# Performance work log

Hardware: AMD Instinct MI355X
Metric: run time of the kernel (lower is better)

## Reference

```python
import jax, jax.numpy as jnp
import numpy as np

NUM_HEADS = 16


def setup_inputs() -> dict:
    rng = jax.random.key(0)
    ks = jax.random.split(rng, 11)
    T, B, E = 1024, 4, 1024
    s = E ** -0.5  # weight init scale
    return {
        "query": jax.random.normal(ks[0], (T, B, E), jnp.float32),
        "key": jax.random.normal(ks[1], (T, B, E), jnp.float32),
        "value": jax.random.normal(ks[2], (T, B, E), jnp.float32),
        "q_proj_weight": jax.random.normal(ks[3], (E, E), jnp.float32) * s,
        "k_proj_weight1": jax.random.normal(ks[4], (E, E), jnp.float32) * s,
        "k_proj_weight2": jax.random.normal(ks[5], (E, E), jnp.float32) * s,
        "v_proj_weight": jax.random.normal(ks[6], (E, E), jnp.float32) * s,
        "in_proj_bias": jax.random.normal(ks[7], (4 * E,), jnp.float32) * 0.02,
        "out_proj_weight": jax.random.normal(ks[8], (E, E), jnp.float32) * s,
        "out_proj_bias": jax.random.normal(ks[9], (E,), jnp.float32) * 0.02,
        "pi": jax.random.uniform(ks[10], (2, NUM_HEADS), jnp.float32, 0.3, 0.7),
    }


def reference(query, key, value, q_proj_weight, k_proj_weight1, k_proj_weight2,
              v_proj_weight, in_proj_bias, out_proj_weight, out_proj_bias, pi):
    T, Bz, E = query.shape
    H = NUM_HEADS
    hd = E // H
    scaling = hd ** -0.5

    b_q, b_k1, b_k2, b_v = jnp.split(in_proj_bias, 4)
    q = query @ q_proj_weight.T + b_q
    k1 = key @ k_proj_weight1.T + b_k1
    k2 = key @ k_proj_weight2.T + b_k2
    v = value @ v_proj_weight.T + b_v

    def heads(x):  # (S, B, E) -> (B*H, S, hd)
        S = x.shape[0]
        return x.reshape(S, Bz * H, hd).transpose(1, 0, 2)

    q, k1, k2, v = heads(q), heads(k1), heads(k2), heads(v)

    def sqdist(a, b):  # (B*H, Nt, hd), (B*H, Ns, hd) -> (B*H, Nt, Ns)
        a2 = jnp.sum(a * a, axis=-1)
        b2 = jnp.sum(b * b, axis=-1)
        ab = jnp.einsum('btd,bsd->bts', a, b)
        return a2[:, :, None] + b2[:, None, :] - 2.0 * ab

    e1 = jnp.exp(-scaling / 2.0 * sqdist(q, k1))
    e2 = jnp.exp(-3.0 * scaling / 2.0 * sqdist(q, k2))

    pi1 = jnp.clip(jnp.abs(pi[0]), 1e-6, 2.0)  # (H,)
    pi2 = jnp.clip(jnp.abs(pi[1]), 1e-6, 2.0)

    Nt, Ns = e1.shape[1], e1.shape[2]
    attn = (e1.reshape(Bz, H, Nt, Ns) * pi1[None, :, None, None]
            + e2.reshape(Bz, H, Nt, Ns) * pi2[None, :, None, None])
    attn = attn.reshape(Bz * H, Nt, Ns)
    attn = attn / (jnp.sum(attn, axis=-1, keepdims=True) + 1e-6)

    out = jnp.einsum('bts,bsd->btd', attn, v)        # (B*H, Nt, hd)
    out = out.transpose(1, 0, 2).reshape(T, Bz, E)   # (T, B, E)
    return out @ out_proj_weight.T + out_proj_bias
```

## Files before the change

### kernel.cpp

```cpp
#include <hip/hip_runtime.h>
#include <hip/hip_bf16.h>

#define T_DIM 1024
#define B_DIM 4
#define E_DIM 1024
#define H_DIM 16
#define HD    64
#define M_DIM (T_DIM * B_DIM)

typedef __hip_bfloat16 bf16;
typedef __bf16 bf16x8 __attribute__((ext_vector_type(8)));
typedef __bf16 bf16x4 __attribute__((ext_vector_type(4)));
typedef float  f32x4  __attribute__((ext_vector_type(4)));

#define P4S ((size_t)M_DIM * E_DIM)
#define P1S ((size_t)E_DIM * E_DIM)

__global__ __launch_bounds__(256) void cvt_all(
    const float* __restrict__ q, const float* __restrict__ k,
    const float* __restrict__ v, const float* __restrict__ w0,
    const float* __restrict__ w1, const float* __restrict__ w2,
    const float* __restrict__ w3, const float* __restrict__ w4,
    __bf16* __restrict__ dst)
{
  size_t i = ((size_t)blockIdx.x * 256 + threadIdx.x) * 8;
  const float* src;
  size_t off;
  if (i < P4S)            { src = q; off = i; }
  else if (i < 2 * P4S)   { src = k; off = i - P4S; }
  else if (i < 3 * P4S)   { src = v; off = i - 2 * P4S; }
  else {
    size_t j = i - 3 * P4S;
    int wsel = (int)(j >> 20);
    off = j & (P1S - 1);
    const float* ws[5] = {w0, w1, w2, w3, w4};
    src = ws[wsel];
  }
  float4 a = *(const float4*)(src + off);
  float4 b = *(const float4*)(src + off + 4);
  bf16x8 o;
  o[0] = (__bf16)a.x; o[1] = (__bf16)a.y; o[2] = (__bf16)a.z; o[3] = (__bf16)a.w;
  o[4] = (__bf16)b.x; o[5] = (__bf16)b.y; o[6] = (__bf16)b.z; o[7] = (__bf16)b.w;
  *(bf16x8*)(dst + i) = o;
}

__device__ __forceinline__ void load_lds16(const __bf16* g, __bf16* l) {
  __builtin_amdgcn_global_load_lds(
      (__attribute__((address_space(1))) void*)(void*)g,
      (__attribute__((address_space(3))) void*)l, 16, 0, 0);
}

template <typename TO>
__device__ __forceinline__ void gemm_body(
    const __bf16* __restrict__ X, const __bf16* __restrict__ W,
    const float* __restrict__ bias, TO* __restrict__ C,
    int bm, int bn, int Ndim, int Kdim, __bf16* As, __bf16* Bs)
{
  const int tid  = threadIdx.x;
  const int lane = tid & 63;
  const int wave = tid >> 6;
  const int wy = (wave >> 1) * 64;
  const int wx = (wave & 1) * 64;
  const int mrow = lane & 15, quad = lane >> 4;

  const int srow = tid >> 2;
  const int ke   = (tid & 3) * 8;
  const __bf16* gA0 = X + (size_t)(bm + srow)      * Kdim + ke;
  const __bf16* gA1 = X + (size_t)(bm + srow + 64) * Kdim + ke;
  const __bf16* gB0 = W + (size_t)(bn + srow)      * Kdim + ke;
  const __bf16* gB1 = W + (size_t)(bn + srow + 64) * Kdim + ke;
  __bf16* lA0 = As + tid * 8;
  __bf16* lA1 = As + (tid + 256) * 8;
  __bf16* lB0 = Bs + tid * 8;
  __bf16* lB1 = Bs + (tid + 256) * 8;

  f32x4 acc[4][4];
#pragma unroll
  for (int i = 0; i < 4; ++i)
#pragma unroll
    for (int j = 0; j < 4; ++j) acc[i][j] = (f32x4)0.0f;

  for (int k0 = 0; k0 < Kdim; k0 += 32) {
    __syncthreads();
    load_lds16(gA0 + k0, lA0);
    load_lds16(gA1 + k0, lA1);
    load_lds16(gB0 + k0, lB0);
    load_lds16(gB1 + k0, lB1);
    __syncthreads();
    bf16x8 af[4], bf[4];
#pragma unroll
    for (int i = 0; i < 4; ++i)
      af[i] = *(const bf16x8*)(As + (wy + i * 16 + mrow) * 32 + quad * 8);
#pragma unroll
    for (int j = 0; j < 4; ++j)
      bf[j] = *(const bf16x8*)(Bs + (wx + j * 16 + mrow) * 32 + quad * 8);
#pragma unroll
    for (int i = 0; i < 4; ++i)
#pragma unroll
      for (int j = 0; j < 4; ++j)
        acc[i][j] = __builtin_amdgcn_mfma_f32_16x16x32_bf16(af[i], bf[j], acc[i][j], 0, 0, 0);
  }

#pragma unroll
  for (int j = 0; j < 4; ++j) {
    int col = bn + wx + j * 16 + mrow;
    float bc = bias[col];
#pragma unroll
    for (int i = 0; i < 4; ++i) {
      int rbase = bm + wy + i * 16 + quad * 4;
#pragma unroll
      for (int r = 0; r < 4; ++r)
        C[(size_t)(rbase + r) * Ndim + col] = (TO)(acc[i][j][r] + bc);
    }
  }
}

__global__ __launch_bounds__(256) void proj_gemm4(
    const __bf16* __restrict__ xbase, const __bf16* __restrict__ wbase,
    const float* __restrict__ bin, __bf16* __restrict__ cbase)
{
  __shared__ __bf16 As[128 * 32];
  __shared__ __bf16 Bs[128 * 32];
  const int z = blockIdx.z;
  const __bf16* X = xbase + ((z == 0) ? 0 : (z == 3) ? 2 * P4S : P4S);
  const __bf16* W = wbase + (size_t)z * P1S;
  const float* bias = bin + z * E_DIM;
  __bf16* C = cbase + (size_t)z * P4S;
  gemm_body<__bf16>(X, W, bias, C, blockIdx.x * 128, blockIdx.y * 128,
                    E_DIM, E_DIM, As, Bs);
}

__global__ __launch_bounds__(256) void out_gemm(
    const __bf16* __restrict__ X, const __bf16* __restrict__ W,
    const float* __restrict__ bias, float* __restrict__ C)
{
  __shared__ __bf16 As[128 * 32];
  __shared__ __bf16 Bs[128 * 32];
  gemm_body<float>(X, W, bias, C, blockIdx.x * 128, blockIdx.y * 128,
                   E_DIM, E_DIM, As, Bs);
}

__global__ __launch_bounds__(256) void head_norms(
    const __bf16* __restrict__ Qp, const __bf16* __restrict__ K1p,
    const __bf16* __restrict__ K2p, float* __restrict__ qn,
    float* __restrict__ kn1, float* __restrict__ kn2)
{
  int id = blockIdx.x * 256 + threadIdx.x;
  int which = id >> 16;
  int r = id & 65535;
  int bh = r >> 10, t = r & 1023;
  int b = bh >> 4, h = bh & 15;
  const __bf16* src = (which == 0) ? Qp : ((which == 1) ? K1p : K2p);
  float* dst = (which == 0) ? qn : ((which == 1) ? kn1 : kn2);
  const __bf16* p = src + (size_t)(t * 4 + b) * 1024 + h * 64;
  float s = 0.f;
#pragma unroll
  for (int c = 0; c < 8; ++c) {
    bf16x8 v = *(const bf16x8*)(p + c * 8);
#pragma unroll
    for (int j = 0; j < 8; ++j) { float x = (float)v[j]; s += x * x; }
  }
  dst[bh * 1024 + t] = s;
}

__global__ __launch_bounds__(256) void v_transpose(
    const __bf16* __restrict__ Vp, __bf16* __restrict__ Vt_g)
{
  const int bh = blockIdx.x, kt = blockIdx.y;
  const int b = bh >> 4, h = bh & 15;
  const int tid = threadIdx.x;
  __shared__ __bf16 tile[64][88];
  {
    int s = tid >> 2, d0 = (tid & 3) * 16;
    const __bf16* src = Vp + (size_t)((kt * 64 + s) * 4 + b) * 1024 + h * 64 + d0;
    *(bf16x8*)(&tile[s][d0])     = *(const bf16x8*)(src);
    *(bf16x8*)(&tile[s][d0 + 8]) = *(const bf16x8*)(src + 8);
  }
  __syncthreads();
#pragma unroll
  for (int c = 0; c < 2; ++c) {
    int idx = tid * 2 + c;
    int d = idx >> 3, u0 = (idx & 7) * 8;
    bf16x8 o;
#pragma unroll
    for (int i = 0; i < 8; ++i) {
      int u = u0 + i;
      int s = (u & 3) * 16 + (u >> 2);
      o[i] = tile[s][d];
    }
    *(bf16x8*)(Vt_g + ((size_t)bh * 64 + d) * 1024 + kt * 64 + u0) = o;
  }
}

__global__ __launch_bounds__(256, 2) void mgk_attn_mfma(
    const __bf16* __restrict__ Qp, const __bf16* __restrict__ K1p,
    const __bf16* __restrict__ K2p, const __bf16* __restrict__ Vt_g,
    const float* __restrict__ qn_g, const float* __restrict__ kn1_g,
    const float* __restrict__ kn2_g, const float* __restrict__ pi,
    __bf16* __restrict__ AO)
{
  __shared__ __bf16 lds[28672];
  __bf16* Qs  = lds;
  __bf16* K1s = lds + 8192;
  __bf16* K2s = lds + 12288;
  __bf16* Vt  = lds + 16384;
  __bf16* Pl  = lds + 20480;

  const int bh = blockIdx.x, qt = blockIdx.y;
  const int b = bh >> 4, h = bh & 15;
  const int tid = threadIdx.x, lane = tid & 63, w = tid >> 6;
  const int mrow = lane & 15, quad = lane >> 4;

  const float c1 = 0.0625f;
  const float c2 = 0.1875f;
  const float p1 = fminf(fmaxf(fabsf(pi[h]), 1e-6f), 2.0f);
  const float p2 = fminf(fmaxf(fabsf(pi[H_DIM + h]), 1e-6f), 2.0f);
  const int hoff = h * 64;

  f32x4 qnv[2];
#pragma unroll
  for (int i = 0; i < 2; ++i)
    qnv[i] = *(const f32x4*)(qn_g + bh * 1024 + qt * 128 + w * 32 + i * 16 + quad * 4);

#pragma unroll
  for (int wi = 0; wi < 4; ++wi) {
    int window = w * 4 + wi;
    int qr = window * 8 + (lane >> 3), c = lane & 7;
    const __bf16* src = Qp + (size_t)((qt * 128 + qr) * 4 + b) * 1024 + hoff
                        + ((c ^ (qr & 7)) << 3);
    load_lds16(src, Qs + window * 512 + lane * 8);
  }

  f32x4 oacc[2][4];
#pragma unroll
  for (int i = 0; i < 2; ++i)
#pragma unroll
    for (int j = 0; j < 4; ++j) oacc[i][j] = (f32x4)0.0f;
  f32x4 rsl[2] = {(f32x4)0.0f, (f32x4)0.0f};

  for (int kt = 0; kt < 16; ++kt) {
    __syncthreads();
#pragma unroll
    for (int wi = 0; wi < 2; ++wi) {
      int window = w * 2 + wi;
      int kr = window * 8 + (lane >> 3), c = lane & 7;
      size_t srow = (size_t)((kt * 64 + kr) * 4 + b) * 1024 + hoff;
      int off = (c ^ (kr & 7)) << 3;
      load_lds16(K1p + srow + off, K1s + window * 512 + lane * 8);
      load_lds16(K2p + srow + off, K2s + window * 512 + lane * 8);
      load_lds16(Vt_g + ((size_t)bh * 64 + kr) * 1024 + kt * 64 + off,
                 Vt + window * 512 + lane * 8);
    }
    float kn1j[4], kn2j[4];
#pragma unroll
    for (int j = 0; j < 4; ++j) {
      kn1j[j] = kn1_g[bh * 1024 + kt * 64 + j * 16 + mrow];
      kn2j[j] = kn2_g[bh * 1024 + kt * 64 + j * 16 + mrow];
    }
    __syncthreads();

    bf16x8 af[2][2];
#pragma unroll
    for (int i = 0; i < 2; ++i)
#pragma unroll
      for (int kk = 0; kk < 2; ++kk)
        af[i][kk] = *(const bf16x8*)(Qs + (w * 32 + i * 16 + mrow) * 64
                                     + (((kk * 4 + quad) ^ (mrow & 7)) << 3));
    f32x4 acc1[2][4], acc2[2][4];
#pragma unroll
    for (int i = 0; i < 2; ++i)
#pragma unroll
      for (int j = 0; j < 4; ++j) { acc1[i][j] = (f32x4)0.0f; acc2[i][j] = (f32x4)0.0f; }
#pragma unroll
    for (int kk = 0; kk < 2; ++kk)
#pragma unroll
      for (int j = 0; j < 4; ++j) {
        bf16x8 b1f = *(const bf16x8*)(K1s + (j * 16 + mrow) * 64
                                      + (((kk * 4 + quad) ^ (mrow & 7)) << 3));
        bf16x8 b2f = *(const bf16x8*)(K2s + (j * 16 + mrow) * 64
                                      + (((kk * 4 + quad) ^ (mrow & 7)) << 3));
#pragma unroll
        for (int i = 0; i < 2; ++i) {
          acc1[i][j] = __builtin_amdgcn_mfma_f32_16x16x32_bf16(af[i][kk], b1f, acc1[i][j], 0, 0, 0);
          acc2[i][j] = __builtin_amdgcn_mfma_f32_16x16x32_bf16(af[i][kk], b2f, acc2[i][j], 0, 0, 0);
        }
      }

#pragma unroll
    for (int i = 0; i < 2; ++i) {
      f32x4 pv[4];
#pragma unroll
      for (int j = 0; j < 4; ++j) {
        f32x4 p;
#pragma unroll
        for (int r = 0; r < 4; ++r) {
          float arg1 = c1 * (2.0f * acc1[i][j][r] - qnv[i][r] - kn1j[j]);
          float arg2 = c2 * (2.0f * acc2[i][j][r] - qnv[i][r] - kn2j[j]);
          p[r] = p1 * __expf(arg1) + p2 * __expf(arg2);
        }
        pv[j] = p;
        rsl[i] += p;
      }
#pragma unroll
      for (int r = 0; r < 4; ++r) {
        int q = i * 16 + quad * 4 + r;
        bf16x4 pk;
        pk[0] = (__bf16)pv[0][r]; pk[1] = (__bf16)pv[1][r];
        pk[2] = (__bf16)pv[2][r]; pk[3] = (__bf16)pv[3][r];
        int lc = mrow >> 1;
        *(bf16x4*)(Pl + w * 2048 + q * 64 + ((lc ^ (q & 7)) << 3) + (mrow & 1) * 4) = pk;
      }
    }
    __syncthreads();

    bf16x8 pf[2][2];
#pragma unroll
    for (int i = 0; i < 2; ++i)
#pragma unroll
      for (int kk = 0; kk < 2; ++kk)
        pf[i][kk] = *(const bf16x8*)(Pl + w * 2048 + (i * 16 + mrow) * 64
                                     + (((kk * 4 + quad) ^ (mrow & 7)) << 3));
#pragma unroll
    for (int kk = 0; kk < 2; ++kk)
#pragma unroll
      for (int j = 0; j < 4; ++j) {
        bf16x8 vf = *(const bf16x8*)(Vt + (j * 16 + mrow) * 64
                                     + (((kk * 4 + quad) ^ (mrow & 7)) << 3));
#pragma unroll
        for (int i = 0; i < 2; ++i)
          oacc[i][j] = __builtin_amdgcn_mfma_f32_16x16x32_bf16(pf[i][kk], vf, oacc[i][j], 0, 0, 0);
      }
  }

#pragma unroll
  for (int i = 0; i < 2; ++i)
#pragma unroll
    for (int d = 1; d < 16; d <<= 1) {
      f32x4 o;
#pragma unroll
      for (int r = 0; r < 4; ++r) o[r] = __shfl_xor(rsl[i][r], d, 64);
      rsl[i] += o;
    }

#pragma unroll
  for (int i = 0; i < 2; ++i) {
    f32x4 inv;
#pragma unroll
    for (int r = 0; r < 4; ++r) inv[r] = 1.0f / (rsl[i][r] + 1e-6f);
#pragma unroll
    for (int j = 0; j < 4; ++j) {
      int col = hoff + j * 16 + mrow;
#pragma unroll
      for (int r = 0; r < 4; ++r) {
        int t = qt * 128 + w * 32 + i * 16 + quad * 4 + r;
        AO[(size_t)(t * 4 + b) * 1024 + col] = (__bf16)(oacc[i][j][r] * inv[r]);
      }
    }
  }
}

extern "C" void kernel_launch(void* const* d_in, const int* in_sizes, int n_in,
                              void* d_out, int out_size, void* d_ws, size_t ws_size,
                              hipStream_t stream) {
  const float* query = (const float*)d_in[0];
  const float* key   = (const float*)d_in[1];
  const float* value = (const float*)d_in[2];
  const float* Wq    = (const float*)d_in[3];
  const float* Wk1   = (const float*)d_in[4];
  const float* Wk2   = (const float*)d_in[5];
  const float* Wv    = (const float*)d_in[6];
  const float* bin   = (const float*)d_in[7];
  const float* Wo    = (const float*)d_in[8];
  const float* bo    = (const float*)d_in[9];
  const float* pi    = (const float*)d_in[10];
  float* out = (float*)d_out;

  __bf16* qc  = (__bf16*)d_ws;
  __bf16* wq  = qc  + 3 * P4S;
  __bf16* wo  = wq  + 4 * P1S;
  __bf16* Qp  = wq  + 5 * P1S;
  __bf16* K1p = Qp  + P4S;
  __bf16* K2p = K1p + P4S;
  __bf16* Vp  = K2p + P4S;
  __bf16* AO  = Vp  + P4S;
  float*  qn_g  = (float*)(AO + P4S);
  float*  kn1_g = qn_g  + 64 * 1024;
  float*  kn2_g = kn1_g + 64 * 1024;
  __bf16* Vt_g  = qc;

  cvt_all<<<8704, 256, 0, stream>>>(query, key, value, Wq, Wk1, Wk2, Wv, Wo, qc);

  proj_gemm4<<<dim3(M_DIM / 128, E_DIM / 128, 4), 256, 0, stream>>>(qc, wq, bin, Qp);

  head_norms<<<768, 256, 0, stream>>>(Qp, K1p, K2p, qn_g, kn1_g, kn2_g);
  v_transpose<<<dim3(64, 16), 256, 0, stream>>>(Vp, Vt_g);

  mgk_attn_mfma<<<dim3(64, 8), 256, 0, stream>>>(
      Qp, K1p, K2p, Vt_g, qn_g, kn1_g, kn2_g, pi, AO);

  out_gemm<<<dim3(M_DIM / 128, E_DIM / 128), 256, 0, stream>>>(AO, wo, bo, out);
}
```

Measured before the change: 265.1 us.

## Shrink attention query tile to 64 rows, hold Q in registers, use exp2

The attention kernel now handles 64 query rows per block instead of 128, which doubles the grid to 1024 blocks. It keeps each wave's Q fragment in registers instead of staging it in LDS, cutting LDS use from 56KB to 32KB and raising the launch bound to 4 blocks per CU. The exponent math is folded into FMA plus exp2 with precomputed log2e-scaled query-norm terms, and the barrier between writing P and reading it back is removed because each wave uses only its own P region. In exchange, every K1/K2/V tile is loaded from global memory twice as many times overall.

```diff
diff --git a/kernel.cpp b/kernel.cpp
--- a/kernel.cpp
+++ b/kernel.cpp
@@ -192,51 +192,47 @@
   }
 }
 
-__global__ __launch_bounds__(256, 2) void mgk_attn_mfma(
+__global__ __launch_bounds__(256, 4) void mgk_attn_mfma(
     const __bf16* __restrict__ Qp, const __bf16* __restrict__ K1p,
     const __bf16* __restrict__ K2p, const __bf16* __restrict__ Vt_g,
     const float* __restrict__ qn_g, const float* __restrict__ kn1_g,
     const float* __restrict__ kn2_g, const float* __restrict__ pi,
     __bf16* __restrict__ AO)
 {
-  __shared__ __bf16 lds[28672];
-  __bf16* Qs  = lds;
-  __bf16* K1s = lds + 8192;
-  __bf16* K2s = lds + 12288;
-  __bf16* Vt  = lds + 16384;
-  __bf16* Pl  = lds + 20480;
+  __shared__ __bf16 lds[16384];
+  __bf16* K1s = lds;
+  __bf16* K2s = lds + 4096;
+  __bf16* Vt  = lds + 8192;
+  __bf16* Pl  = lds + 12288;
 
   const int bh = blockIdx.x, qt = blockIdx.y;
   const int b = bh >> 4, h = bh & 15;
   const int tid = threadIdx.x, lane = tid & 63, w = tid >> 6;
   const int mrow = lane & 15, quad = lane >> 4;
 
-  const float c1 = 0.0625f;
-  const float c2 = 0.1875f;
+  const float cl1 = 0.0625f * 1.4426950408889634f;
+  const float cl2 = 0.1875f * 1.4426950408889634f;
+  const float L1 = 2.0f * cl1, L2 = 2.0f * cl2;
   const float p1 = fminf(fmaxf(fabsf(pi[h]), 1e-6f), 2.0f);
   const float p2 = fminf(fmaxf(fabsf(pi[H_DIM + h]), 1e-6f), 2.0f);
   const int hoff = h * 64;
 
-  f32x4 qnv[2];
-#pragma unroll
-  for (int i = 0; i < 2; ++i)
-    qnv[i] = *(const f32x4*)(qn_g + bh * 1024 + qt * 128 + w * 32 + i * 16 + quad * 4);
-
-#pragma unroll
-  for (int wi = 0; wi < 4; ++wi) {
-    int window = w * 4 + wi;
-    int qr = window * 8 + (lane >> 3), c = lane & 7;
-    const __bf16* src = Qp + (size_t)((qt * 128 + qr) * 4 + b) * 1024 + hoff
-                        + ((c ^ (qr & 7)) << 3);
-    load_lds16(src, Qs + window * 512 + lane * 8);
-  }
-
-  f32x4 oacc[2][4];
-#pragma unroll
-  for (int i = 0; i < 2; ++i)
-#pragma unroll
-    for (int j = 0; j < 4; ++j) oacc[i][j] = (f32x4)0.0f;
-  f32x4 rsl[2] = {(f32x4)0.0f, (f32x4)0.0f};
+  bf16x8 af[2];
+  {
+    const __bf16* qp = Qp + (size_t)((qt * 64 + w * 16 + mrow) * 4 + b) * 1024
+                       + hoff + quad * 8;
+    af[0] = *(const bf16x8*)(qp);
+    af[1] = *(const bf16x8*)(qp + 32);
+  }
+  f32x4 qnv = *(const f32x4*)(qn_g + bh * 1024 + qt * 64 + w * 16 + quad * 4);
+  f32x4 ncq1, ncq2;
+#pragma unroll
+  for (int r = 0; r < 4; ++r) { ncq1[r] = -cl1 * qnv[r]; ncq2[r] = -cl2 * qnv[r]; }
+
+  f32x4 oacc[4];
+#pragma unroll
+  for (int j = 0; j < 4; ++j) oacc[j] = (f32x4)0.0f;
+  f32x4 rsl = (f32x4)0.0f;
 
   for (int kt = 0; kt < 16; ++kt) {
     __syncthreads();
@@ -259,18 +255,9 @@
     }
     __syncthreads();
 
-    bf16x8 af[2][2];
-#pragma unroll
-    for (int i = 0; i < 2; ++i)
-#pragma unroll
-      for (int kk = 0; kk < 2; ++kk)
-        af[i][kk] = *(const bf16x8*)(Qs + (w * 32 + i * 16 + mrow) * 64
-                                     + (((kk * 4 + quad) ^ (mrow & 7)) << 3));
-    f32x4 acc1[2][4], acc2[2][4];
-#pragma unroll
-    for (int i = 0; i < 2; ++i)
-#pragma unroll
-      for (int j = 0; j < 4; ++j) { acc1[i][j] = (f32x4)0.0f; acc2[i][j] = (f32x4)0.0f; }
+    f32x4 acc1[4], acc2[4];
+#pragma unroll
+    for (int j = 0; j < 4; ++j) { acc1[j] = (f32x4)0.0f; acc2[j] = (f32x4)0.0f; }
 #pragma unroll
     for (int kk = 0; kk < 2; ++kk)
 #pragma unroll
@@ -279,82 +266,66 @@
                                       + (((kk * 4 + quad) ^ (mrow & 7)) << 3));
         bf16x8 b2f = *(const bf16x8*)(K2s + (j * 16 + mrow) * 64
                                       + (((kk * 4 + quad) ^ (mrow & 7)) << 3));
-#pragma unroll
-        for (int i = 0; i < 2; ++i) {
-          acc1[i][j] = __builtin_amdgcn_mfma_f32_16x16x32_bf16(af[i][kk], b1f, acc1[i][j], 0, 0, 0);
-          acc2[i][j] = __builtin_amdgcn_mfma_f32_16x16x32_bf16(af[i][kk], b2f, acc2[i][j], 0, 0, 0);
-        }
+        acc1[j] = __builtin_amdgcn_mfma_f32_16x16x32_bf16(af[kk], b1f, acc1[j], 0, 0, 0);
+        acc2[j] = __builtin_amdgcn_mfma_f32_16x16x32_bf16(af[kk], b2f, acc2[j], 0, 0, 0);
       }
 
-#pragma unroll
-    for (int i = 0; i < 2; ++i) {
-      f32x4 pv[4];
-#pragma unroll
-      for (int j = 0; j < 4; ++j) {
-        f32x4 p;
-#pragma unroll
-        for (int r = 0; r < 4; ++r) {
-          float arg1 = c1 * (2.0f * acc1[i][j][r] - qnv[i][r] - kn1j[j]);
-          float arg2 = c2 * (2.0f * acc2[i][j][r] - qnv[i][r] - kn2j[j]);
-          p[r] = p1 * __expf(arg1) + p2 * __expf(arg2);
-        }
-        pv[j] = p;
-        rsl[i] += p;
+    f32x4 pv[4];
+#pragma unroll
+    for (int j = 0; j < 4; ++j) {
+      f32x4 p;
+#pragma unroll
+      for (int r = 0; r < 4; ++r) {
+        float e1 = __builtin_amdgcn_exp2f(fmaf(L1, acc1[j][r], fmaf(-cl1, kn1j[j], ncq1[r])));
+        float e2 = __builtin_amdgcn_exp2f(fmaf(L2, acc2[j][r], fmaf(-cl2, kn2j[j], ncq2[r])));
+        p[r] = fmaf(p2, e2, p1 * e1);
       }
-#pragma unroll
-      for (int r = 0; r < 4; ++r) {
-        int q = i * 16 + quad * 4 + r;
-        bf16x4 pk;
-        pk[0] = (__bf16)pv[0][r]; pk[1] = (__bf16)pv[1][r];
-        pk[2] = (__bf16)pv[2][r]; pk[3] = (__bf16)pv[3][r];
-        int lc = mrow >> 1;
-        *(bf16x4*)(Pl + w * 2048 + q * 64 + ((lc ^ (q & 7)) << 3) + (mrow & 1) * 4) = pk;
-      }
-    }
-    __syncthreads();
-
-    bf16x8 pf[2][2];
-#pragma unroll
-    for (int i = 0; i < 2; ++i)
-#pragma unroll
-      for (int kk = 0; kk < 2; ++kk)
-        pf[i][kk] = *(const bf16x8*)(Pl + w * 2048 + (i * 16 + mrow) * 64
-                                     + (((kk * 4 + quad) ^ (mrow & 7)) << 3));
+      pv[j] = p;
+      rsl += p;
+    }
+#pragma unroll
+    for (int r = 0; r < 4; ++r) {
+      int q = quad * 4 + r;
+      bf16x4 pk;
+      pk[0] = (__bf16)pv[0][r]; pk[1] = (__bf16)pv[1][r];
+      pk[2] = (__bf16)pv[2][r]; pk[3] = (__bf16)pv[3][r];
+      int lc = mrow >> 1;
+      *(bf16x4*)(Pl + w * 1024 + q * 64 + ((lc ^ (q & 7)) << 3) + (mrow & 1) * 4) = pk;
+    }
+
+    bf16x8 pf[2];
+#pragma unroll
+    for (int kk = 0; kk < 2; ++kk)
+      pf[kk] = *(const bf16x8*)(Pl + w * 1024 + mrow * 64
+                                + (((kk * 4 + quad) ^ (mrow & 7)) << 3));
 #pragma unroll
     for (int kk = 0; kk < 2; ++kk)
 #pragma unroll
       for (int j = 0; j < 4; ++j) {
         bf16x8 vf = *(const bf16x8*)(Vt + (j * 16 + mrow) * 64
                                      + (((kk * 4 + quad) ^ (mrow & 7)) << 3));
-#pragma unroll
-        for (int i = 0; i < 2; ++i)
-          oacc[i][j] = __builtin_amdgcn_mfma_f32_16x16x32_bf16(pf[i][kk], vf, oacc[i][j], 0, 0, 0);
+        oacc[j] = __builtin_amdgcn_mfma_f32_16x16x32_bf16(pf[kk], vf, oacc[j], 0, 0, 0);
       }
   }
 
 #pragma unroll
-  for (int i = 0; i < 2; ++i)
-#pragma unroll
-    for (int d = 1; d < 16; d <<= 1) {
-      f32x4 o;
-#pragma unroll
-      for (int r = 0; r < 4; ++r) o[r] = __shfl_xor(rsl[i][r], d, 64);
-      rsl[i] += o;
-    }
-
-#pragma unroll
-  for (int i = 0; i < 2; ++i) {
-    f32x4 inv;
-#pragma unroll
-    for (int r = 0; r < 4; ++r) inv[r] = 1.0f / (rsl[i][r] + 1e-6f);
-#pragma unroll
-    for (int j = 0; j < 4; ++j) {
-      int col = hoff + j * 16 + mrow;
-#pragma unroll
-      for (int r = 0; r < 4; ++r) {
-        int t = qt * 128 + w * 32 + i * 16 + quad * 4 + r;
-        AO[(size_t)(t * 4 + b) * 1024 + col] = (__bf16)(oacc[i][j][r] * inv[r]);
-      }
+  for (int d = 1; d < 16; d <<= 1) {
+    f32x4 o;
+#pragma unroll
+    for (int r = 0; r < 4; ++r) o[r] = __shfl_xor(rsl[r], d, 64);
+    rsl += o;
+  }
+
+  f32x4 inv;
+#pragma unroll
+  for (int r = 0; r < 4; ++r) inv[r] = 1.0f / (rsl[r] + 1e-6f);
+#pragma unroll
+  for (int j = 0; j < 4; ++j) {
+    int col = hoff + j * 16 + mrow;
+#pragma unroll
+    for (int r = 0; r < 4; ++r) {
+      int t = qt * 64 + w * 16 + quad * 4 + r;
+      AO[(size_t)(t * 4 + b) * 1024 + col] = (__bf16)(oacc[j][r] * inv[r]);
     }
   }
 }
@@ -395,7 +366,7 @@
   head_norms<<<768, 256, 0, stream>>>(Qp, K1p, K2p, qn_g, kn1_g, kn2_g);
   v_transpose<<<dim3(64, 16), 256, 0, stream>>>(Vp, Vt_g);
 
-  mgk_attn_mfma<<<dim3(64, 8), 256, 0, stream>>>(
+  mgk_attn_mfma<<<dim3(64, 16), 256, 0, stream>>>(
       Qp, K1p, K2p, Vt_g, qn_g, kn1_g, kn2_g, pi, AO);
 
   out_gemm<<<dim3(M_DIM / 128, E_DIM / 128), 256, 0, stream>>>(AO, wo, bo, out);
```

Result: no change. 270.4 us (+2.0%).
